# Optimization experiments

Hardware: AMD Instinct MI355X
Metric: run time of the kernel (lower is better)

Reference implementation:

```python
import jax, jax.numpy as jnp
import numpy as np

SEQ_LEN = 4096
D_IN = 1024
D_OUT = 1024


def setup_inputs() -> dict:
    key = jax.random.key(0)
    k_x, k_q, k_k, k_v = jax.random.split(key, 4)
    s = 1.0 / np.sqrt(D_IN)
    return {
        "x": jax.random.normal(k_x, (SEQ_LEN, D_IN), dtype=jnp.float32),
        "W_query": jax.random.normal(k_q, (D_IN, D_OUT), dtype=jnp.float32) * s,
        "W_key": jax.random.normal(k_k, (D_IN, D_OUT), dtype=jnp.float32) * s,
        "W_value": jax.random.normal(k_v, (D_IN, D_OUT), dtype=jnp.float32) * s,
    }


def reference(x, W_query, W_key, W_value):
    # QKV projections (Linear without bias): [S, d_out]
    q = x @ W_query
    k = x @ W_key
    v = x @ W_value
    # Full S x S score matrix, causal mask, scaled softmax
    scores = q @ k.T  # [S, S]
    seq_len = x.shape[0]
    causal = jnp.tril(jnp.ones((seq_len, seq_len), dtype=bool))
    scores = jnp.where(causal, scores, -jnp.inf)
    scale = 1.0 / jnp.sqrt(jnp.asarray(k.shape[-1], dtype=scores.dtype))
    attn = jax.nn.softmax(scores * scale, axis=-1)
    return attn @ v  # [S, d_out]
```

## Files before the change

### kernel.cpp

```cpp
#include <hip/hip_runtime.h>
#include <math.h>

#define SEQ 4096
#define DIM 1024

typedef unsigned short u16;
typedef __attribute__((ext_vector_type(8))) short short8;
typedef __attribute__((ext_vector_type(4))) float floatx4;
typedef __attribute__((ext_vector_type(4))) unsigned short us4;

__device__ __forceinline__ float bf2f(u16 u) {
    union { unsigned int i; float f; } c; c.i = ((unsigned int)u) << 16; return c.f;
}
__device__ __forceinline__ u16 f2bf(float f) {
    union { float f; unsigned int i; } c; c.f = f;
    return (u16)((c.i + 0x7fffu + ((c.i >> 16) & 1u)) >> 16);
}
__device__ __forceinline__ void gload_lds16(const u16* g, u16* l) {
    __builtin_amdgcn_global_load_lds((const __attribute__((address_space(1))) void*)g,
                                     (__attribute__((address_space(3))) void*)l, 16, 0, 0);
}

template <int MODE>
__global__ __launch_bounds__(256) void gemm_nt(const u16* __restrict__ A,
                                               const u16* __restrict__ B,
                                               void* __restrict__ Cv,
                                               u16* __restrict__ VtOut,
                                               float* __restrict__ Lsum,
                                               int lda, int ldb, int ldc, int Kdim,
                                               float scale0) {
    int row0, col0, kbeg = 0, kend = Kdim;
    if (MODE == 1) {
        const int t = blockIdx.x;
        int by = (int)((sqrtf(8.0f * t + 1.0f) - 1.0f) * 0.5f);
        while ((by + 1) * (by + 2) / 2 <= t) ++by;
        while (by * (by + 1) / 2 > t) --by;
        const int bx = t - by * (by + 1) / 2;
        row0 = by * 128;
        col0 = bx * 128;
    } else if (MODE == 2) {
        col0 = blockIdx.x * 128;
        const int u = blockIdx.y;
        int r, c;
        if (u < 32)      { c = 0; r = u; }
        else if (u < 56) { c = 1; r = u - 24; }
        else if (u < 72) { c = 2; r = u - 40; }
        else             { c = 3; r = u - 48; }
        row0 = r * 128;
        kbeg = c << 10;
        kend = min(kbeg + 1024, row0 + 128);
    } else {
        row0 = blockIdx.y * 128;
        col0 = blockIdx.x * 128;
    }

    __shared__ u16 As[3][4096];
    __shared__ u16 Bs[3][4096];

    const int tid  = threadIdx.x;
    const int wave = tid >> 6;
    const int lane = tid & 63;
    const int wm = wave & 1;
    const int wn = wave >> 1;

    const int s0 = wave * 128 + lane;
    const int s1 = s0 + 64;
    const int r0s = s0 >> 2, q0s = ((s0 & 3) ^ ((s0 >> 3) & 3)) * 8;
    const int r1s = s1 >> 2, q1s = ((s1 & 3) ^ ((s1 >> 3) & 3)) * 8;
    const u16* aP0 = A + (size_t)(row0 + r0s) * lda + kbeg + q0s;
    const u16* aP1 = A + (size_t)(row0 + r1s) * lda + kbeg + q1s;
    const u16* bP0 = B + (size_t)(col0 + r0s) * ldb + kbeg + q0s;
    const u16* bP1 = B + (size_t)(col0 + r1s) * ldb + kbeg + q1s;
    const int l0 = wave * 1024;

    floatx4 acc[4][4] = {};
    const int niter = (kend - kbeg) >> 5;
    const int frow = lane & 15;
    const int xq = (((lane >> 4) ^ ((frow >> 1) & 3))) * 8;

    gload_lds16(aP0, &As[0][l0]);
    gload_lds16(aP1, &As[0][l0 + 512]);
    gload_lds16(bP0, &Bs[0][l0]);
    gload_lds16(bP1, &Bs[0][l0 + 512]);
    aP0 += 32; aP1 += 32; bP0 += 32; bP1 += 32;
    gload_lds16(aP0, &As[1][l0]);
    gload_lds16(aP1, &As[1][l0 + 512]);
    gload_lds16(bP0, &Bs[1][l0]);
    gload_lds16(bP1, &Bs[1][l0 + 512]);
    aP0 += 32; aP1 += 32; bP0 += 32; bP1 += 32;

    auto compute_tile = [&](int c) {
        short8 af[4], bfr[4];
#pragma unroll
        for (int t = 0; t < 4; ++t) {
            af[t]  = *(const short8*)&As[c][(wm * 64 + t * 16 + frow) * 32 + xq];
            bfr[t] = *(const short8*)&Bs[c][(wn * 64 + t * 16 + frow) * 32 + xq];
        }
#pragma unroll
        for (int mt = 0; mt < 4; ++mt)
#pragma unroll
            for (int nt = 0; nt < 4; ++nt)
                acc[mt][nt] = __builtin_amdgcn_mfma_f32_16x16x32_bf16(
                    af[mt], bfr[nt], acc[mt][nt], 0, 0, 0);
    };

    int cur = 0, pre = 2;
    for (int it = 0; it < niter - 2; ++it) {
        asm volatile("s_waitcnt vmcnt(4)\n\ts_barrier" ::: "memory");
        short8 af[4], bfr[4];
#pragma unroll
        for (int t = 0; t < 4; ++t) {
            af[t]  = *(const short8*)&As[cur][(wm * 64 + t * 16 + frow) * 32 + xq];
            bfr[t] = *(const short8*)&Bs[cur][(wn * 64 + t * 16 + frow) * 32 + xq];
        }
        gload_lds16(aP0, &As[pre][l0]);
        gload_lds16(aP1, &As[pre][l0 + 512]);
        gload_lds16(bP0, &Bs[pre][l0]);
        gload_lds16(bP1, &Bs[pre][l0 + 512]);
        aP0 += 32; aP1 += 32; bP0 += 32; bP1 += 32;
#pragma unroll
        for (int mt = 0; mt < 4; ++mt)
#pragma unroll
            for (int nt = 0; nt < 4; ++nt)
                acc[mt][nt] = __builtin_amdgcn_mfma_f32_16x16x32_bf16(
                    af[mt], bfr[nt], acc[mt][nt], 0, 0, 0);
        cur = (cur == 2) ? 0 : cur + 1;
        pre = (pre == 2) ? 0 : pre + 1;
    }
    asm volatile("s_waitcnt vmcnt(4)\n\ts_barrier" ::: "memory");
    compute_tile(cur);
    cur = (cur == 2) ? 0 : cur + 1;
    asm volatile("s_waitcnt vmcnt(0)\n\ts_barrier" ::: "memory");
    compute_tile(cur);

    const int cr = (lane >> 4) * 4;
    const int cc = lane & 15;
    if (MODE == 1) {
        u16* dst = (u16*)Cv;
#pragma unroll
        for (int mt = 0; mt < 4; ++mt) {
#pragma unroll
            for (int r = 0; r < 4; ++r) {
                const int grow = row0 + wm * 64 + mt * 16 + cr + r;
                float rowsum = 0.f;
#pragma unroll
                for (int nt = 0; nt < 4; ++nt) {
                    const int gcol = col0 + wn * 64 + nt * 16 + cc;
                    const float e = (gcol <= grow) ? __expf(acc[mt][nt][r]) : 0.f;
                    rowsum += e;
                    dst[(size_t)grow * ldc + gcol] = f2bf(e);
                }
                rowsum += __shfl_xor(rowsum, 1);
                rowsum += __shfl_xor(rowsum, 2);
                rowsum += __shfl_xor(rowsum, 4);
                rowsum += __shfl_xor(rowsum, 8);
                if (cc == 0) atomicAdd(&Lsum[grow], rowsum);
            }
        }
    } else if (MODE == 2) {
        float* O = (float*)Cv;
#pragma unroll
        for (int mt = 0; mt < 4; ++mt)
#pragma unroll
            for (int r = 0; r < 4; ++r) {
                const int grow = row0 + wm * 64 + mt * 16 + cr + r;
                const float invl = 1.0f / Lsum[grow];
#pragma unroll
                for (int nt = 0; nt < 4; ++nt) {
                    const int col = col0 + wn * 64 + nt * 16 + cc;
                    atomicAdd(&O[(size_t)grow * ldc + col], acc[mt][nt][r] * invl);
                }
            }
    } else if (MODE == 0 && col0 >= 2048) {
#pragma unroll
        for (int mt = 0; mt < 4; ++mt)
#pragma unroll
            for (int nt = 0; nt < 4; ++nt) {
                const int row = row0 + wm * 64 + mt * 16 + cr;
                const int col = (col0 - 2048) + wn * 64 + nt * 16 + cc;
                us4 o = { f2bf(acc[mt][nt][0]), f2bf(acc[mt][nt][1]),
                          f2bf(acc[mt][nt][2]), f2bf(acc[mt][nt][3]) };
                *(us4*)&VtOut[(size_t)col * SEQ + row] = o;
            }
    } else {
        u16* dst = (u16*)Cv;
        const float sc = (col0 < 1024) ? scale0 : 1.0f;
#pragma unroll
        for (int mt = 0; mt < 4; ++mt)
#pragma unroll
            for (int nt = 0; nt < 4; ++nt)
#pragma unroll
                for (int r = 0; r < 4; ++r) {
                    const int row = row0 + wm * 64 + mt * 16 + cr + r;
                    const int col = col0 + wn * 64 + nt * 16 + cc;
                    dst[(size_t)row * ldc + col] = f2bf(acc[mt][nt][r] * sc);
                }
    }
}

__global__ __launch_bounds__(256) void prep(const float* __restrict__ x,
                                            const float* __restrict__ W0,
                                            const float* __restrict__ W1,
                                            const float* __restrict__ W2,
                                            u16* __restrict__ xb,
                                            u16* __restrict__ Wt,
                                            float* __restrict__ O,
                                            float* __restrict__ Lsum) {
    __shared__ float tile[32][33];
    const int b = blockIdx.x;
    const int tid = threadIdx.x;
    if (b < 4096) {
        const size_t i = ((size_t)b * 256 + tid) * 4;
        const float4 v = *(const float4*)(x + i);
        us4 o = { f2bf(v.x), f2bf(v.y), f2bf(v.z), f2bf(v.w) };
        *(us4*)(xb + i) = o;
    } else if (b < 7168) {
        const int t = b - 4096;
        const int z = t >> 10;
        const int idx = t & 1023;
        const float* W = (z == 0) ? W0 : (z == 1) ? W1 : W2;
        u16* out = Wt + (size_t)z * DIM * DIM;
        const int bx = (idx & 31) * 32;
        const int by = (idx >> 5) * 32;
        const int tx = tid & 31;
        const int ty = (tid >> 5) * 4;
#pragma unroll
        for (int r = 0; r < 4; ++r)
            tile[ty + r][tx] = W[(size_t)(by + ty + r) * DIM + bx + tx];
        __syncthreads();
#pragma unroll
        for (int r = 0; r < 4; ++r)
            out[(size_t)(bx + ty + r) * DIM + by + tx] = f2bf(tile[tx][ty + r]);
    } else {
        const int t = b - 7168;
        const size_t i = ((size_t)t * 256 + tid) * 4;
        *(float4*)(O + i) = make_float4(0.f, 0.f, 0.f, 0.f);
        if (t < 4) *(float4*)(Lsum + (size_t)(t * 256 + tid) * 4) =
            make_float4(0.f, 0.f, 0.f, 0.f);
    }
}

extern "C" void kernel_launch(void* const* d_in, const int* in_sizes, int n_in,
                              void* d_out, int out_size, void* d_ws, size_t ws_size,
                              hipStream_t stream) {
    const float* x  = (const float*)d_in[0];
    const float* Wq = (const float*)d_in[1];
    const float* Wk = (const float*)d_in[2];
    const float* Wv = (const float*)d_in[3];

    u16* xb    = (u16*)d_ws;
    u16* Wt    = xb  + (size_t)SEQ * DIM;
    u16* QK    = Wt  + (size_t)3072 * DIM;
    u16* Vt    = QK  + (size_t)SEQ * 2048;
    u16* E     = Vt  + (size_t)DIM * SEQ;
    float* Lsum = (float*)(E + (size_t)SEQ * SEQ);

    prep<<<8192, 256, 0, stream>>>(x, Wq, Wk, Wv, xb, Wt, (float*)d_out, Lsum);

    gemm_nt<0><<<dim3(24, 32), 256, 0, stream>>>(
        xb, Wt, QK, Vt, nullptr, DIM, DIM, 2048, DIM, 0.03125f);

    gemm_nt<1><<<528, 256, 0, stream>>>(
        QK, QK + 1024, E, nullptr, Lsum, 2048, 2048, SEQ, DIM, 1.0f);

    gemm_nt<2><<<dim3(8, 80), 256, 0, stream>>>(
        E, Vt, d_out, nullptr, Lsum, SEQ, SEQ, DIM, SEQ, 1.0f);
}
```

Measured before the change: 197.7 us.

## Split GEMM kernel and use 512-thread blocks for attention GEMMs

Splits the templated GEMM into a QKV projection kernel and an attention kernel. The attention kernel runs 8 waves per 128x128 tile with a 4x2 accumulator per wave, and waves are split so half load A and half load B. Launch bounds of (512,4) aim for more resident waves to hide latency. The grid order changes: the scores pass launches a full 32x32 grid and exits above-diagonal blocks early, and the PV pass swaps grid axes. The risks are more barrier cost per tile, fewer MFMAs per LDS read, and idle launched blocks in the scores pass.

```diff
diff --git a/kernel.cpp b/kernel.cpp
--- a/kernel.cpp
+++ b/kernel.cpp
@@ -21,38 +21,12 @@
                                      (__attribute__((address_space(3))) void*)l, 16, 0, 0);
 }
 
-template <int MODE>
-__global__ __launch_bounds__(256) void gemm_nt(const u16* __restrict__ A,
-                                               const u16* __restrict__ B,
-                                               void* __restrict__ Cv,
-                                               u16* __restrict__ VtOut,
-                                               float* __restrict__ Lsum,
-                                               int lda, int ldb, int ldc, int Kdim,
-                                               float scale0) {
-    int row0, col0, kbeg = 0, kend = Kdim;
-    if (MODE == 1) {
-        const int t = blockIdx.x;
-        int by = (int)((sqrtf(8.0f * t + 1.0f) - 1.0f) * 0.5f);
-        while ((by + 1) * (by + 2) / 2 <= t) ++by;
-        while (by * (by + 1) / 2 > t) --by;
-        const int bx = t - by * (by + 1) / 2;
-        row0 = by * 128;
-        col0 = bx * 128;
-    } else if (MODE == 2) {
-        col0 = blockIdx.x * 128;
-        const int u = blockIdx.y;
-        int r, c;
-        if (u < 32)      { c = 0; r = u; }
-        else if (u < 56) { c = 1; r = u - 24; }
-        else if (u < 72) { c = 2; r = u - 40; }
-        else             { c = 3; r = u - 48; }
-        row0 = r * 128;
-        kbeg = c << 10;
-        kend = min(kbeg + 1024, row0 + 128);
-    } else {
-        row0 = blockIdx.y * 128;
-        col0 = blockIdx.x * 128;
-    }
+__global__ __launch_bounds__(256) void gemm_qkv(const u16* __restrict__ A,
+                                                const u16* __restrict__ B,
+                                                u16* __restrict__ QK,
+                                                u16* __restrict__ VtOut) {
+    const int row0 = blockIdx.x * 128;
+    const int col0 = blockIdx.y * 128;
 
     __shared__ u16 As[3][4096];
     __shared__ u16 Bs[3][4096];
@@ -67,14 +41,14 @@
     const int s1 = s0 + 64;
     const int r0s = s0 >> 2, q0s = ((s0 & 3) ^ ((s0 >> 3) & 3)) * 8;
     const int r1s = s1 >> 2, q1s = ((s1 & 3) ^ ((s1 >> 3) & 3)) * 8;
-    const u16* aP0 = A + (size_t)(row0 + r0s) * lda + kbeg + q0s;
-    const u16* aP1 = A + (size_t)(row0 + r1s) * lda + kbeg + q1s;
-    const u16* bP0 = B + (size_t)(col0 + r0s) * ldb + kbeg + q0s;
-    const u16* bP1 = B + (size_t)(col0 + r1s) * ldb + kbeg + q1s;
+    const u16* aP0 = A + (size_t)(row0 + r0s) * DIM + q0s;
+    const u16* aP1 = A + (size_t)(row0 + r1s) * DIM + q1s;
+    const u16* bP0 = B + (size_t)(col0 + r0s) * DIM + q0s;
+    const u16* bP1 = B + (size_t)(col0 + r1s) * DIM + q1s;
     const int l0 = wave * 1024;
 
     floatx4 acc[4][4] = {};
-    const int niter = (kend - kbeg) >> 5;
+    const int niter = DIM >> 5;
     const int frow = lane & 15;
     const int xq = (((lane >> 4) ^ ((frow >> 1) & 3))) * 8;
 
@@ -135,8 +109,144 @@
 
     const int cr = (lane >> 4) * 4;
     const int cc = lane & 15;
-    if (MODE == 1) {
-        u16* dst = (u16*)Cv;
+    if (col0 >= 2048) {
+#pragma unroll
+        for (int mt = 0; mt < 4; ++mt)
+#pragma unroll
+            for (int nt = 0; nt < 4; ++nt) {
+                const int row = row0 + wm * 64 + mt * 16 + cr;
+                const int col = (col0 - 2048) + wn * 64 + nt * 16 + cc;
+                us4 o = { f2bf(acc[mt][nt][0]), f2bf(acc[mt][nt][1]),
+                          f2bf(acc[mt][nt][2]), f2bf(acc[mt][nt][3]) };
+                *(us4*)&VtOut[(size_t)col * SEQ + row] = o;
+            }
+    } else {
+        const float sc = (col0 < 1024) ? 0.03125f : 1.0f;
+#pragma unroll
+        for (int mt = 0; mt < 4; ++mt)
+#pragma unroll
+            for (int nt = 0; nt < 4; ++nt)
+#pragma unroll
+                for (int r = 0; r < 4; ++r) {
+                    const int row = row0 + wm * 64 + mt * 16 + cr + r;
+                    const int col = col0 + wn * 64 + nt * 16 + cc;
+                    QK[(size_t)row * 2048 + col] = f2bf(acc[mt][nt][r] * sc);
+                }
+    }
+}
+
+template <int SCORES>
+__global__ __launch_bounds__(512, 4) void gemm_att(const u16* __restrict__ A,
+                                                   const u16* __restrict__ B,
+                                                   void* __restrict__ Cv,
+                                                   float* __restrict__ Lsum,
+                                                   int lda, int ldb) {
+    int row0, col0, kbeg = 0, kend;
+    if (SCORES) {
+        col0 = blockIdx.x * 128;
+        row0 = blockIdx.y * 128;
+        if (col0 > row0) return;
+        kend = DIM;
+    } else {
+        const int u = blockIdx.x;
+        col0 = blockIdx.y * 128;
+        int r, c;
+        if (u < 32)      { c = 0; r = u; }
+        else if (u < 56) { c = 1; r = u - 24; }
+        else if (u < 72) { c = 2; r = u - 40; }
+        else             { c = 3; r = u - 48; }
+        row0 = r * 128;
+        kbeg = c << 10;
+        kend = min(kbeg + 1024, row0 + 128);
+    }
+
+    __shared__ u16 As[3][4096];
+    __shared__ u16 Bs[3][4096];
+
+    const int tid  = threadIdx.x;
+    const int wave = tid >> 6;
+    const int lane = tid & 63;
+    const int wm = wave & 1;
+    const int wn = wave >> 1;
+
+    const int sw = wave & 3;
+    const int s0 = sw * 128 + lane;
+    const int s1 = s0 + 64;
+    const int r0s = s0 >> 2, q0s = ((s0 & 3) ^ ((s0 >> 3) & 3)) * 8;
+    const int r1s = s1 >> 2, q1s = ((s1 & 3) ^ ((s1 >> 3) & 3)) * 8;
+    const bool isA = wave < 4;
+    const u16* p0 = isA ? A + (size_t)(row0 + r0s) * lda + kbeg + q0s
+                        : B + (size_t)(col0 + r0s) * ldb + kbeg + q0s;
+    const u16* p1 = isA ? A + (size_t)(row0 + r1s) * lda + kbeg + q1s
+                        : B + (size_t)(col0 + r1s) * ldb + kbeg + q1s;
+    const int o0 = s0 * 8;
+    const int o1 = o0 + 512;
+
+    floatx4 acc[4][2] = {};
+    const int niter = (kend - kbeg) >> 5;
+    const int frow = lane & 15;
+    const int xq = (((lane >> 4) ^ ((frow >> 1) & 3))) * 8;
+
+    {
+        u16* d0 = isA ? &As[0][0] : &Bs[0][0];
+        gload_lds16(p0, d0 + o0);
+        gload_lds16(p1, d0 + o1);
+        p0 += 32; p1 += 32;
+        u16* d1 = isA ? &As[1][0] : &Bs[1][0];
+        gload_lds16(p0, d1 + o0);
+        gload_lds16(p1, d1 + o1);
+        p0 += 32; p1 += 32;
+    }
+
+    auto compute_tile = [&](int c) {
+        short8 af[4], bfr[2];
+#pragma unroll
+        for (int t = 0; t < 4; ++t)
+            af[t] = *(const short8*)&As[c][(wm * 64 + t * 16 + frow) * 32 + xq];
+#pragma unroll
+        for (int t = 0; t < 2; ++t)
+            bfr[t] = *(const short8*)&Bs[c][(wn * 32 + t * 16 + frow) * 32 + xq];
+#pragma unroll
+        for (int mt = 0; mt < 4; ++mt)
+#pragma unroll
+            for (int nt = 0; nt < 2; ++nt)
+                acc[mt][nt] = __builtin_amdgcn_mfma_f32_16x16x32_bf16(
+                    af[mt], bfr[nt], acc[mt][nt], 0, 0, 0);
+    };
+
+    int cur = 0, pre = 2;
+    for (int it = 0; it < niter - 2; ++it) {
+        asm volatile("s_waitcnt vmcnt(2)\n\ts_barrier" ::: "memory");
+        short8 af[4], bfr[2];
+#pragma unroll
+        for (int t = 0; t < 4; ++t)
+            af[t] = *(const short8*)&As[cur][(wm * 64 + t * 16 + frow) * 32 + xq];
+#pragma unroll
+        for (int t = 0; t < 2; ++t)
+            bfr[t] = *(const short8*)&Bs[cur][(wn * 32 + t * 16 + frow) * 32 + xq];
+        u16* dp = isA ? &As[pre][0] : &Bs[pre][0];
+        gload_lds16(p0, dp + o0);
+        gload_lds16(p1, dp + o1);
+        p0 += 32; p1 += 32;
+#pragma unroll
+        for (int mt = 0; mt < 4; ++mt)
+#pragma unroll
+            for (int nt = 0; nt < 2; ++nt)
+                acc[mt][nt] = __builtin_amdgcn_mfma_f32_16x16x32_bf16(
+                    af[mt], bfr[nt], acc[mt][nt], 0, 0, 0);
+        cur = (cur == 2) ? 0 : cur + 1;
+        pre = (pre == 2) ? 0 : pre + 1;
+    }
+    asm volatile("s_waitcnt vmcnt(2)\n\ts_barrier" ::: "memory");
+    compute_tile(cur);
+    cur = (cur == 2) ? 0 : cur + 1;
+    asm volatile("s_waitcnt vmcnt(0)\n\ts_barrier" ::: "memory");
+    compute_tile(cur);
+
+    const int cr = (lane >> 4) * 4;
+    const int cc = lane & 15;
+    if (SCORES) {
+        u16* E = (u16*)Cv;
 #pragma unroll
         for (int mt = 0; mt < 4; ++mt) {
 #pragma unroll
@@ -144,11 +254,11 @@
                 const int grow = row0 + wm * 64 + mt * 16 + cr + r;
                 float rowsum = 0.f;
 #pragma unroll
-                for (int nt = 0; nt < 4; ++nt) {
-                    const int gcol = col0 + wn * 64 + nt * 16 + cc;
+                for (int nt = 0; nt < 2; ++nt) {
+                    const int gcol = col0 + wn * 32 + nt * 16 + cc;
                     const float e = (gcol <= grow) ? __expf(acc[mt][nt][r]) : 0.f;
                     rowsum += e;
-                    dst[(size_t)grow * ldc + gcol] = f2bf(e);
+                    E[(size_t)grow * SEQ + gcol] = f2bf(e);
                 }
                 rowsum += __shfl_xor(rowsum, 1);
                 rowsum += __shfl_xor(rowsum, 2);
@@ -157,7 +267,7 @@
                 if (cc == 0) atomicAdd(&Lsum[grow], rowsum);
             }
         }
-    } else if (MODE == 2) {
+    } else {
         float* O = (float*)Cv;
 #pragma unroll
         for (int mt = 0; mt < 4; ++mt)
@@ -166,35 +276,11 @@
                 const int grow = row0 + wm * 64 + mt * 16 + cr + r;
                 const float invl = 1.0f / Lsum[grow];
 #pragma unroll
-                for (int nt = 0; nt < 4; ++nt) {
-                    const int col = col0 + wn * 64 + nt * 16 + cc;
-                    atomicAdd(&O[(size_t)grow * ldc + col], acc[mt][nt][r] * invl);
+                for (int nt = 0; nt < 2; ++nt) {
+                    const int col = col0 + wn * 32 + nt * 16 + cc;
+                    atomicAdd(&O[(size_t)grow * DIM + col], acc[mt][nt][r] * invl);
                 }
             }
-    } else if (MODE == 0 && col0 >= 2048) {
-#pragma unroll
-        for (int mt = 0; mt < 4; ++mt)
-#pragma unroll
-            for (int nt = 0; nt < 4; ++nt) {
-                const int row = row0 + wm * 64 + mt * 16 + cr;
-                const int col = (col0 - 2048) + wn * 64 + nt * 16 + cc;
-                us4 o = { f2bf(acc[mt][nt][0]), f2bf(acc[mt][nt][1]),
-                          f2bf(acc[mt][nt][2]), f2bf(acc[mt][nt][3]) };
-                *(us4*)&VtOut[(size_t)col * SEQ + row] = o;
-            }
-    } else {
-        u16* dst = (u16*)Cv;
-        const float sc = (col0 < 1024) ? scale0 : 1.0f;
-#pragma unroll
-        for (int mt = 0; mt < 4; ++mt)
-#pragma unroll
-            for (int nt = 0; nt < 4; ++nt)
-#pragma unroll
-                for (int r = 0; r < 4; ++r) {
-                    const int row = row0 + wm * 64 + mt * 16 + cr + r;
-                    const int col = col0 + wn * 64 + nt * 16 + cc;
-                    dst[(size_t)row * ldc + col] = f2bf(acc[mt][nt][r] * sc);
-                }
     }
 }
 
@@ -248,21 +334,20 @@
     const float* Wk = (const float*)d_in[2];
     const float* Wv = (const float*)d_in[3];
 
-    u16* xb    = (u16*)d_ws;
-    u16* Wt    = xb  + (size_t)SEQ * DIM;
-    u16* QK    = Wt  + (size_t)3072 * DIM;
-    u16* Vt    = QK  + (size_t)SEQ * 2048;
-    u16* E     = Vt  + (size_t)DIM * SEQ;
+    u16* xb   = (u16*)d_ws;
+    u16* Wt   = xb + (size_t)SEQ * DIM;
+    u16* QK   = Wt + (size_t)3072 * DIM;
+    u16* Vt   = QK + (size_t)SEQ * 2048;
+    u16* E    = Vt + (size_t)DIM * SEQ;
     float* Lsum = (float*)(E + (size_t)SEQ * SEQ);
 
     prep<<<8192, 256, 0, stream>>>(x, Wq, Wk, Wv, xb, Wt, (float*)d_out, Lsum);
 
-    gemm_nt<0><<<dim3(24, 32), 256, 0, stream>>>(
-        xb, Wt, QK, Vt, nullptr, DIM, DIM, 2048, DIM, 0.03125f);
-
-    gemm_nt<1><<<528, 256, 0, stream>>>(
-        QK, QK + 1024, E, nullptr, Lsum, 2048, 2048, SEQ, DIM, 1.0f);
-
-    gemm_nt<2><<<dim3(8, 80), 256, 0, stream>>>(
-        E, Vt, d_out, nullptr, Lsum, SEQ, SEQ, DIM, SEQ, 1.0f);
-}
+    gemm_qkv<<<dim3(32, 24), 256, 0, stream>>>(xb, Wt, QK, Vt);
+
+    gemm_att<1><<<dim3(32, 32), 512, 0, stream>>>(
+        QK, QK + 1024, E, Lsum, 2048, 2048);
+
+    gemm_att<0><<<dim3(80, 8), 512, 0, stream>>>(
+        E, Vt, d_out, Lsum, SEQ, SEQ);
+}
```

Result: slower. 209.3 us (+5.9%).
